# Performance work log

Hardware: AMD Instinct MI355X
Metric: run time of the kernel (lower is better)

## Reference

```python
import jax, jax.numpy as jnp
from jax import lax
import numpy as np

B, L = 256, 4096
H, RL, RH = 128, 2, 32   # num_hiddens, residual layers, residual hiddens
K, D = 512, 64           # codebook size, embedding dim
CC = 0.25                # commitment cost


def conv1d(x, w, b=None, stride=1, pad=0, circular=False):
    # x: (N,C,L), w: (O,I,k)
    if circular and pad > 0:
        x = jnp.pad(x, ((0, 0), (0, 0), (pad, pad)), mode='wrap')
        pad = 0
    y = lax.conv_general_dilated(x, w, (stride,), [(pad, pad)],
                                 dimension_numbers=('NCH', 'OIH', 'NCH'))
    return y if b is None else y + b[None, :, None]


def convt1d(x, w, b):
    # PyTorch ConvTranspose1d(k=4, s=2, p=1); w: (I,O,4). out_len = 2*L.
    wt = jnp.flip(jnp.swapaxes(w, 0, 1), -1)  # (O,I,4)
    y = lax.conv_general_dilated(x, wt, (1,), [(2, 2)], lhs_dilation=(2,),
                                 dimension_numbers=('NCH', 'OIH', 'NCH'))
    return y + b[None, :, None]


def res_stack(x, w1s, w2s):
    for i in range(w1s.shape[0]):
        h = conv1d(jax.nn.relu(x), w1s[i], None, 1, 1, circular=True)
        h = conv1d(jax.nn.relu(h), w2s[i], None, 1, 0)
        x = x + h
    return jax.nn.relu(x)


def setup_inputs() -> dict:
    key = jax.random.key(0)
    ks = iter(jax.random.split(key, 64))

    def w(*shape):
        fan_in = int(np.prod(shape[1:]))
        return jax.random.normal(next(ks), shape, jnp.float32) / np.sqrt(fan_in)

    def bias(n):
        return jax.random.uniform(next(ks), (n,), jnp.float32, -0.05, 0.05)

    inp = {'x': jax.random.normal(next(ks), (B, 1, L), jnp.float32)}
    # Encoder
    inp['enc_c1_w'] = w(H // 2, 1, 4);      inp['enc_c1_b'] = bias(H // 2)
    inp['enc_c2_w'] = w(H, H // 2, 4);      inp['enc_c2_b'] = bias(H)
    inp['enc_c3_w'] = w(H, H, 4);           inp['enc_c3_b'] = bias(H)
    inp['enc_c4_w'] = w(H, H, 4);           inp['enc_c4_b'] = bias(H)
    inp['enc_cf_w'] = w(H, H, 3);           inp['enc_cf_b'] = bias(H)
    inp['enc_res_w1'] = w(RL, RH, H, 3)
    inp['enc_res_w2'] = w(RL, H, RH, 1)
    # pre-VQ 1x1 conv
    inp['prevq_w'] = w(D, H, 1);            inp['prevq_b'] = bias(D)
    # codebook: uniform(-1/K, 1/K) as in source
    inp['emb'] = jax.random.uniform(next(ks), (K, D), jnp.float32, -1.0 / K, 1.0 / K)
    # Decoder
    inp['dec_init_w'] = w(H, D, 3);         inp['dec_init_b'] = bias(H)
    inp['dec_res_w1'] = w(RL, RH, H, 3)
    inp['dec_res_w2'] = w(RL, H, RH, 1)
    inp['ct0_w'] = w(H, H, 4);              inp['ct0_b'] = bias(H)
    inp['ct1_w'] = w(H, H, 4);              inp['ct1_b'] = bias(H)
    inp['ct2_w'] = w(H, H // 2, 4);         inp['ct2_b'] = bias(H // 2)
    inp['ct3_w'] = w(H // 2, 1, 4);         inp['ct3_b'] = bias(1)
    return inp


def _forward(x, enc_c1_w, enc_c1_b, enc_c2_w, enc_c2_b, enc_c3_w, enc_c3_b,
             enc_c4_w, enc_c4_b, enc_cf_w, enc_cf_b, enc_res_w1, enc_res_w2,
             prevq_w, prevq_b, emb, dec_init_w, dec_init_b, dec_res_w1,
             dec_res_w2, ct0_w, ct0_b, ct1_w, ct1_b, ct2_w, ct2_b, ct3_w, ct3_b):
    sg = lax.stop_gradient
    relu = jax.nn.relu
    # ---- Encoder (circular padding) ----
    z = relu(conv1d(x, enc_c1_w, enc_c1_b, 2, 1, circular=True))
    z = relu(conv1d(z, enc_c2_w, enc_c2_b, 2, 1, circular=True))
    z = relu(conv1d(z, enc_c3_w, enc_c3_b, 2, 1, circular=True))
    z = relu(conv1d(z, enc_c4_w, enc_c4_b, 2, 1, circular=True))
    z = conv1d(z, enc_cf_w, enc_cf_b, 1, 1, circular=True)
    z = res_stack(z, enc_res_w1, enc_res_w2)
    z = conv1d(z, prevq_w, prevq_b, 1, 0)        # (B, D, T)
    # ---- Vector quantizer ----
    z_t = jnp.transpose(z, (0, 2, 1))            # (B, T, D)
    flat = z_t.reshape(-1, D)                    # (BT, D)
    dist = (jnp.sum(flat ** 2, axis=1, keepdims=True)
            + jnp.sum(emb ** 2, axis=1)
            - 2.0 * flat @ emb.T)                # (BT, K)
    idx = jnp.argmin(dist, axis=1)               # (BT,)
    enc = jax.nn.one_hot(idx, K, dtype=flat.dtype)
    q = (enc @ emb).reshape(z_t.shape)           # (B, T, D)
    e_loss = jnp.mean((sg(q) - z_t) ** 2)
    q_loss = jnp.mean((q - sg(z_t)) ** 2)
    loss = q_loss + CC * e_loss
    q_st = z_t + sg(q - z_t)                     # straight-through
    avg = jnp.mean(enc, axis=0)
    perplexity = jnp.exp(-jnp.sum(avg * jnp.log(avg + 1e-10)))
    quantized = jnp.transpose(q_st, (0, 2, 1))   # (B, D, T)
    # ---- Decoder ----
    h = conv1d(quantized, dec_init_w, dec_init_b, 1, 1)
    h = res_stack(h, dec_res_w1, dec_res_w2)
    h = relu(convt1d(h, ct0_w, ct0_b))
    h = relu(convt1d(h, ct1_w, ct1_b))
    h = relu(convt1d(h, ct2_w, ct2_b))
    x_recon = convt1d(h, ct3_w, ct3_b)           # (B, 1, L)
    return loss, x_recon, perplexity


def reference(x, enc_c1_w, enc_c1_b, enc_c2_w, enc_c2_b, enc_c3_w, enc_c3_b,
              enc_c4_w, enc_c4_b, enc_cf_w, enc_cf_b, enc_res_w1, enc_res_w2,
              prevq_w, prevq_b, emb, dec_init_w, dec_init_b, dec_res_w1,
              dec_res_w2, ct0_w, ct0_b, ct1_w, ct1_b, ct2_w, ct2_b, ct3_w, ct3_b):
    return _forward(x, enc_c1_w, enc_c1_b, enc_c2_w, enc_c2_b, enc_c3_w,
                    enc_c3_b, enc_c4_w, enc_c4_b, enc_cf_w, enc_cf_b,
                    enc_res_w1, enc_res_w2, prevq_w, prevq_b, emb,
                    dec_init_w, dec_init_b, dec_res_w1, dec_res_w2,
                    ct0_w, ct0_b, ct1_w, ct1_b, ct2_w, ct2_b, ct3_w, ct3_b)
```

## Files before the change

### kernel.cpp

```cpp
#include <hip/hip_runtime.h>

#define DEVI __device__ __forceinline__

typedef __bf16 bf16x8 __attribute__((ext_vector_type(8)));
typedef float f32x4 __attribute__((ext_vector_type(4)));

DEVI ushort f2b(float f) {
  uint b = __float_as_uint(f);
  uint r = (b + 0x7FFFu + ((b >> 16) & 1u)) >> 16;
  return (ushort)r;
}
DEVI float b2f(ushort u) { return __uint_as_float(((uint)u) << 16); }

struct PrepArgs {
  int nw;
  int tot[20];
  const float* src[20];
  ushort* dst[20];
  int ci[20], co[20], sco[20], sci[20], sk[20];
};

__global__ __launch_bounds__(256)
void prep_all(PrepArgs a, int total) {
  int i = blockIdx.x * 256 + threadIdx.x;
  if (i >= total) return;
  int w = 0;
  while (i >= a.tot[w]) { i -= a.tot[w]; ++w; }
  const int li = i;
  const int CI = a.ci[w];
  int ciX = i % CI;
  int rest = i / CI;
  int coX = rest % a.co[w];
  int k = rest / a.co[w];
  a.dst[w][li] = f2b(a.src[w][coX * a.sco[w] + ciX * a.sci[w] + k * a.sk[w]]);
}

__global__ __launch_bounds__(256)
void enc1_bf(const float* __restrict__ x, const float* __restrict__ w1,
             const float* __restrict__ b1, ushort* __restrict__ out) {
  __shared__ float xl[516];
  __shared__ float w1s[256];
  __shared__ float b1s[64];
  const int n = blockIdx.x >> 3;
  const int t0 = (blockIdx.x & 7) << 8;
  const int tid = threadIdx.x;
  const float* xb = x + ((size_t)n << 12);
  for (int j = tid; j < 514; j += 256)
    xl[j] = xb[(2 * t0 - 1 + j + 4096) & 4095];
  if (tid < 256) w1s[tid] = w1[tid];
  if (tid < 64) b1s[tid] = b1[tid];
  __syncthreads();

  const int oct = tid & 7;
  float4 w4[8];
  float bs[8];
  #pragma unroll
  for (int e = 0; e < 8; ++e) {
    w4[e] = *reinterpret_cast<const float4*>(&w1s[(oct * 8 + e) * 4]);
    bs[e] = b1s[oct * 8 + e];
  }
  ushort* ob = out + (((size_t)n * 2048 + t0) << 6) + tid * 8;
  #pragma unroll
  for (int it = 0; it < 8; ++it) {
    const int tl = it * 32 + (tid >> 3);
    const float x0 = xl[2 * tl], x1 = xl[2 * tl + 1], x2 = xl[2 * tl + 2], x3 = xl[2 * tl + 3];
    uint pack[4];
    #pragma unroll
    for (int h = 0; h < 4; ++h) {
      float s0 = fmaf(w4[2 * h].x, x0, fmaf(w4[2 * h].y, x1,
                 fmaf(w4[2 * h].z, x2, fmaf(w4[2 * h].w, x3, bs[2 * h]))));
      float s1 = fmaf(w4[2 * h + 1].x, x0, fmaf(w4[2 * h + 1].y, x1,
                 fmaf(w4[2 * h + 1].z, x2, fmaf(w4[2 * h + 1].w, x3, bs[2 * h + 1]))));
      pack[h] = (uint)f2b(fmaxf(s0, 0.0f)) | ((uint)f2b(fmaxf(s1, 0.0f)) << 16);
    }
    *reinterpret_cast<uint4*>(ob + it * 2048) = uint4{pack[0], pack[1], pack[2], pack[3]};
  }
}

template<int CI, int CO, int K, int S, bool CIRC, bool GATHER, int NT, int WAVES_CO>
__global__ __launch_bounds__(256)
void conv_mfma(const ushort* __restrict__ in, const ushort* __restrict__ wb,
               const float* __restrict__ bias, const ushort* __restrict__ resid,
               ushort* __restrict__ out, const int* __restrict__ gidx,
               int Tin, int in_relu, int out_relu) {
  constexpr int PAD = (K > 1) ? 1 : 0;
  constexpr int TT = NT * 16;
  constexpr int SPAN = S * (TT - 1) + K;
  constexpr int CIG = CI / 8;
  constexpr int COT = CO / 16;
  constexpr int WCOT = COT / WAVES_CO;
  constexpr int WAVES_T = 4 / WAVES_CO;
  constexpr int WTT = NT / WAVES_T;
  constexpr int KSH = (S == 2) ? 1 : 0;
  static_assert(CI % 32 == 0 && COT % WAVES_CO == 0 && NT % WAVES_T == 0, "");

  __shared__ __align__(16) ushort xs[SPAN * CI];

  const int Tout = Tin / S;
  const int tilesPerB = Tout / TT;
  const int n = blockIdx.x / tilesPerB;
  const int t0 = (blockIdx.x % tilesPerB) * TT;
  const int tid = threadIdx.x;
  const int wid = tid >> 6, lane = tid & 63;
  const int l15 = lane & 15, l4 = lane >> 4;

  const int t_in0 = S * t0 - PAD;
  const ushort* inb = GATHER ? in : in + (size_t)n * Tin * CI;
  for (int i = tid; i < SPAN * CIG; i += 256) {
    int t = i / CIG, g = i - (i / CIG) * CIG;
    int tg = t_in0 + t;
    uint4 v;
    if (CIRC) {
      tg = (tg < 0) ? tg + Tin : (tg >= Tin ? tg - Tin : tg);
      v = *reinterpret_cast<const uint4*>(inb + (size_t)tg * CI + g * 8);
    } else if (GATHER) {
      if ((unsigned)tg < (unsigned)Tin) {
        int id = gidx[n * Tin + tg];
        v = *reinterpret_cast<const uint4*>(inb + (size_t)id * CI + g * 8);
      } else
        v = uint4{0, 0, 0, 0};
    } else {
      if ((unsigned)tg < (unsigned)Tin)
        v = *reinterpret_cast<const uint4*>(inb + (size_t)tg * CI + g * 8);
      else
        v = uint4{0, 0, 0, 0};
    }
    if (in_relu) {
      ushort* pv = reinterpret_cast<ushort*>(&v);
      #pragma unroll
      for (int e = 0; e < 8; ++e) pv[e] = (pv[e] & 0x8000) ? 0 : pv[e];
    }
    *reinterpret_cast<uint4*>(&xs[t * CI + ((g ^ ((t >> KSH) & (CIG - 1))) * 8)]) = v;
  }
  __syncthreads();

  const int wco = wid % WAVES_CO;
  const int wt = wid / WAVES_CO;
  const int co_base = wco * WCOT * 16;
  const int t_base = wt * WTT * 16;

  f32x4 acc[WTT][WCOT] = {};

  for (int cc = 0; cc < CI / 32; ++cc) {
    bf16x8 bk[K][WCOT];
    #pragma unroll
    for (int k = 0; k < K; ++k)
      #pragma unroll
      for (int c = 0; c < WCOT; ++c)
        bk[k][c] = __builtin_bit_cast(bf16x8, *reinterpret_cast<const uint4*>(
            wb + (size_t)((k * CO + co_base + c * 16 + l15)) * CI + cc * 32 + l4 * 8));
    #pragma unroll
    for (int k = 0; k < K; ++k) {
      #pragma unroll
      for (int tt2 = 0; tt2 < WTT; ++tt2) {
        int trow = S * (t_base + tt2 * 16 + l15) + k;
        int g = cc * 4 + l4;
        bf16x8 afr = __builtin_bit_cast(bf16x8, *reinterpret_cast<const uint4*>(
            &xs[trow * CI + ((g ^ ((trow >> KSH) & (CIG - 1))) * 8)]));
        #pragma unroll
        for (int c = 0; c < WCOT; ++c)
          acc[tt2][c] = __builtin_amdgcn_mfma_f32_16x16x32_bf16(afr, bk[k][c], acc[tt2][c], 0, 0, 0);
      }
    }
  }

  float bv[WCOT];
  #pragma unroll
  for (int c = 0; c < WCOT; ++c)
    bv[c] = bias ? bias[co_base + c * 16 + l15] : 0.0f;
  ushort* outb = out + (size_t)n * Tout * CO;
  const ushort* resb = resid ? resid + (size_t)n * Tout * CO : nullptr;
  #pragma unroll
  for (int tt2 = 0; tt2 < WTT; ++tt2)
    #pragma unroll
    for (int c = 0; c < WCOT; ++c)
      #pragma unroll
      for (int r = 0; r < 4; ++r) {
        int t = t0 + t_base + tt2 * 16 + 4 * l4 + r;
        int co = co_base + c * 16 + l15;
        float v = acc[tt2][c][r] + bv[c];
        if (resb) v += b2f(resb[(size_t)t * CO + co]);
        if (out_relu) v = fmaxf(v, 0.0f);
        outb[(size_t)t * CO + co] = f2b(v);
      }
}

__global__ __launch_bounds__(256)
void res_mfma(const ushort* __restrict__ in, const ushort* __restrict__ wb1,
              const ushort* __restrict__ wb2, ushort* __restrict__ out) {
  constexpr int CI = 128, CIG = 16;
  constexpr int TT = 64, SPAN = 66, Tin = 256;
  __shared__ __align__(16) ushort xs[SPAN * CI];
  __shared__ __align__(16) ushort hs[TT][40];
  const int n = blockIdx.x >> 2;
  const int t0 = (blockIdx.x & 3) * TT;
  const int tid = threadIdx.x;
  const int wid = tid >> 6, lane = tid & 63;
  const int l15 = lane & 15, l4 = lane >> 4;
  const int t_in0 = t0 - 1;
  const ushort* inb = in + (size_t)n * Tin * CI;

  for (int i = tid; i < SPAN * CIG; i += 256) {
    int t = i >> 4, g = i & 15;
    int tg = t_in0 + t;
    tg = (tg < 0) ? tg + Tin : (tg >= Tin ? tg - Tin : tg);
    uint4 v = *reinterpret_cast<const uint4*>(inb + (size_t)tg * CI + g * 8);
    ushort* pv = reinterpret_cast<ushort*>(&v);
    #pragma unroll
    for (int e = 0; e < 8; ++e) pv[e] = (pv[e] & 0x8000) ? 0 : pv[e];
    *reinterpret_cast<uint4*>(&xs[t * CI + ((g ^ (t & 15)) * 8)]) = v;
  }
  __syncthreads();

  {
    f32x4 acc[2] = {};
    for (int cc = 0; cc < 4; ++cc)
      #pragma unroll
      for (int k = 0; k < 3; ++k) {
        bf16x8 bfr[2];
        #pragma unroll
        for (int c = 0; c < 2; ++c)
          bfr[c] = __builtin_bit_cast(bf16x8, *reinterpret_cast<const uint4*>(
              wb1 + (size_t)((k * 32 + c * 16 + l15)) * CI + cc * 32 + l4 * 8));
        int trow = wid * 16 + l15 + k;
        int g = cc * 4 + l4;
        bf16x8 afr = __builtin_bit_cast(bf16x8, *reinterpret_cast<const uint4*>(
            &xs[trow * CI + ((g ^ (trow & 15)) * 8)]));
        acc[0] = __builtin_amdgcn_mfma_f32_16x16x32_bf16(afr, bfr[0], acc[0], 0, 0, 0);
        acc[1] = __builtin_amdgcn_mfma_f32_16x16x32_bf16(afr, bfr[1], acc[1], 0, 0, 0);
      }
    #pragma unroll
    for (int c = 0; c < 2; ++c)
      #pragma unroll
      for (int r = 0; r < 4; ++r) {
        float v = acc[c][r];
        hs[wid * 16 + l4 * 4 + r][c * 16 + l15] = (v > 0.0f) ? f2b(v) : (ushort)0;
      }
  }
  __syncthreads();

  {
    bf16x8 afr = *reinterpret_cast<const bf16x8*>(&hs[wid * 16 + l15][l4 * 8]);
    f32x4 acc[8];
    #pragma unroll
    for (int c = 0; c < 8; ++c) {
      bf16x8 bfr = __builtin_bit_cast(bf16x8, *reinterpret_cast<const uint4*>(
          wb2 + (size_t)(c * 16 + l15) * 32 + l4 * 8));
      f32x4 z = {};
      acc[c] = __builtin_amdgcn_mfma_f32_16x16x32_bf16(afr, bfr, z, 0, 0, 0);
    }
    ushort* outb = out + (size_t)n * Tin * CI;
    #pragma unroll
    for (int c = 0; c < 8; ++c)
      #pragma unroll
      for (int r = 0; r < 4; ++r) {
        int t = t0 + wid * 16 + l4 * 4 + r;
        int co = c * 16 + l15;
        float v = acc[c][r] + b2f(inb[(size_t)t * CI + co]);
        outb[(size_t)t * CI + co] = f2b(v);
      }
  }
}

template<int CO>
__global__ __launch_bounds__(256)
void convt_mfma(const ushort* __restrict__ in, const ushort* __restrict__ wb,
                const float* __restrict__ bias, ushort* __restrict__ out,
                int Tin, int in_relu, int out_relu) {
  constexpr int CI = 128, CIG = 16;
  constexpr int NT = 4, TT = 64;
  constexpr int SPAN = TT + 2;
  constexpr int COT = CO / 16;
  constexpr int WCOT = (COT + 3) / 4;
  constexpr int WAVES_CO = COT / WCOT;
  constexpr int WTT = NT;

  __shared__ __align__(16) ushort xs[SPAN * CI];

  const int Tout = 2 * Tin;
  const int tilesPerB = Tin / TT;
  const int n = blockIdx.x / tilesPerB;
  const int tp0 = (blockIdx.x % tilesPerB) * TT;
  const int tid = threadIdx.x;
  const int wid = tid >> 6, lane = tid & 63;
  const int l15 = lane & 15, l4 = lane >> 4;

  const int t_in0 = tp0 - 1;
  const ushort* inb = in + (size_t)n * Tin * CI;
  for (int i = tid; i < SPAN * CIG; i += 256) {
    int t = i >> 4, g = i & 15;
    int tg = t_in0 + t;
    uint4 v;
    if ((unsigned)tg < (unsigned)Tin)
      v = *reinterpret_cast<const uint4*>(inb + (size_t)tg * CI + g * 8);
    else
      v = uint4{0, 0, 0, 0};
    if (in_relu) {
      ushort* pv = reinterpret_cast<ushort*>(&v);
      #pragma unroll
      for (int e = 0; e < 8; ++e) pv[e] = (pv[e] & 0x8000) ? 0 : pv[e];
    }
    *reinterpret_cast<uint4*>(&xs[t * CI + ((g ^ (t & 15)) * 8)]) = v;
  }
  __syncthreads();

  const int wco = wid % WAVES_CO;
  const int co_base = wco * WCOT * 16;

  f32x4 accE[WTT][WCOT] = {};
  f32x4 accO[WTT][WCOT] = {};

  for (int cc = 0; cc < 4; ++cc) {
    bf16x8 bk[4][WCOT];
    #pragma unroll
    for (int k = 0; k < 4; ++k)
      #pragma unroll
      for (int c = 0; c < WCOT; ++c)
        bk[k][c] = __builtin_bit_cast(bf16x8, *reinterpret_cast<const uint4*>(
            wb + (size_t)((k * CO + co_base + c * 16 + l15)) * CI + cc * 32 + l4 * 8));
    #pragma unroll
    for (int tt2 = 0; tt2 < WTT; ++tt2) {
      int lt = tt2 * 16 + l15 + 1;
      int g = cc * 4 + l4;
      bf16x8 a0 = __builtin_bit_cast(bf16x8, *reinterpret_cast<const uint4*>(
          &xs[lt * CI + ((g ^ (lt & 15)) * 8)]));
      bf16x8 am = __builtin_bit_cast(bf16x8, *reinterpret_cast<const uint4*>(
          &xs[(lt - 1) * CI + ((g ^ ((lt - 1) & 15)) * 8)]));
      bf16x8 ap = __builtin_bit_cast(bf16x8, *reinterpret_cast<const uint4*>(
          &xs[(lt + 1) * CI + ((g ^ ((lt + 1) & 15)) * 8)]));
      #pragma unroll
      for (int c = 0; c < WCOT; ++c) {
        accE[tt2][c] = __builtin_amdgcn_mfma_f32_16x16x32_bf16(a0, bk[1][c], accE[tt2][c], 0, 0, 0);
        accE[tt2][c] = __builtin_amdgcn_mfma_f32_16x16x32_bf16(am, bk[3][c], accE[tt2][c], 0, 0, 0);
        accO[tt2][c] = __builtin_amdgcn_mfma_f32_16x16x32_bf16(ap, bk[0][c], accO[tt2][c], 0, 0, 0);
        accO[tt2][c] = __builtin_amdgcn_mfma_f32_16x16x32_bf16(a0, bk[2][c], accO[tt2][c], 0, 0, 0);
      }
    }
  }

  float bv[WCOT];
  #pragma unroll
  for (int c = 0; c < WCOT; ++c) bv[c] = bias[co_base + c * 16 + l15];
  ushort* outb = out + (size_t)n * Tout * CO;
  #pragma unroll
  for (int tt2 = 0; tt2 < WTT; ++tt2)
    #pragma unroll
    for (int c = 0; c < WCOT; ++c)
      #pragma unroll
      for (int r = 0; r < 4; ++r) {
        int tp = tp0 + tt2 * 16 + 4 * l4 + r;
        int co = co_base + c * 16 + l15;
        float vE = accE[tt2][c][r] + bv[c];
        float vO = accO[tt2][c][r] + bv[c];
        if (out_relu) { vE = fmaxf(vE, 0.0f); vO = fmaxf(vO, 0.0f); }
        outb[(size_t)(2 * tp) * CO + co] = f2b(vE);
        outb[(size_t)(2 * tp + 1) * CO + co] = f2b(vO);
      }
}

__global__ __launch_bounds__(256)
void ct23_mfma(const ushort* __restrict__ in, const ushort* __restrict__ wb,
               const float* __restrict__ bias, const float* __restrict__ w3,
               const float* __restrict__ b3, float* __restrict__ out) {
  constexpr int CI = 128, CO = 64, CIG = 16;
  constexpr int TT = 64, SPAN = 66, Tin = 1024;
  __shared__ __align__(16) ushort xs[SPAN * CI];
  __shared__ ushort ys[64 * 134];
  __shared__ float w3s[256];

  const int n = blockIdx.x >> 4;
  const int tp0 = (blockIdx.x & 15) * TT;
  const int tid = threadIdx.x;
  const int wid = tid >> 6, lane = tid & 63;
  const int l15 = lane & 15, l4 = lane >> 4;
  const int t_in0 = tp0 - 1;
  const ushort* inb = in + (size_t)n * Tin * CI;

  if (tid < 256) w3s[tid] = w3[tid];
  for (int i = tid; i < SPAN * CIG; i += 256) {
    int t = i >> 4, g = i & 15;
    int tg = t_in0 + t;
    uint4 v;
    if ((unsigned)tg < (unsigned)Tin)
      v = *reinterpret_cast<const uint4*>(inb + (size_t)tg * CI + g * 8);
    else
      v = uint4{0, 0, 0, 0};
    *reinterpret_cast<uint4*>(&xs[t * CI + ((g ^ (t & 15)) * 8)]) = v;
  }
  __syncthreads();

  const int co_base = wid * 16;
  f32x4 accE[4] = {}, accO[4] = {};
  f32x4 hO = {}, hE = {};

  for (int cc = 0; cc < 4; ++cc) {
    bf16x8 bk[4];
    #pragma unroll
    for (int k = 0; k < 4; ++k)
      bk[k] = __builtin_bit_cast(bf16x8, *reinterpret_cast<const uint4*>(
          wb + (size_t)((k * CO + co_base + l15)) * CI + cc * 32 + l4 * 8));
    const int g = cc * 4 + l4;
    auto rd = [&](int lt) -> bf16x8 {
      return __builtin_bit_cast(bf16x8, *reinterpret_cast<const uint4*>(
          &xs[lt * CI + ((g ^ (lt & 15)) * 8)]));
    };
    #pragma unroll
    for (int tt2 = 0; tt2 < 4; ++tt2) {
      int lt = tt2 * 16 + l15 + 1;
      bf16x8 a0 = rd(lt), am = rd(lt - 1), ap = rd(lt + 1);
      accE[tt2] = __builtin_amdgcn_mfma_f32_16x16x32_bf16(a0, bk[1], accE[tt2], 0, 0, 0);
      accE[tt2] = __builtin_amdgcn_mfma_f32_16x16x32_bf16(am, bk[3], accE[tt2], 0, 0, 0);
      accO[tt2] = __builtin_amdgcn_mfma_f32_16x16x32_bf16(ap, bk[0], accO[tt2], 0, 0, 0);
      accO[tt2] = __builtin_amdgcn_mfma_f32_16x16x32_bf16(a0, bk[2], accO[tt2], 0, 0, 0);
    }
    bf16x8 h0 = rd(0), h1 = rd(1), h64 = rd(64), h65 = rd(65);
    hO = __builtin_amdgcn_mfma_f32_16x16x32_bf16(h1, bk[0], hO, 0, 0, 0);
    hO = __builtin_amdgcn_mfma_f32_16x16x32_bf16(h0, bk[2], hO, 0, 0, 0);
    hE = __builtin_amdgcn_mfma_f32_16x16x32_bf16(h65, bk[1], hE, 0, 0, 0);
    hE = __builtin_amdgcn_mfma_f32_16x16x32_bf16(h64, bk[3], hE, 0, 0, 0);
  }

  const float bv = bias[co_base + l15];
  ushort* yrow = &ys[(co_base + l15) * 134];
  #pragma unroll
  for (int tt2 = 0; tt2 < 4; ++tt2)
    #pragma unroll
    for (int r = 0; r < 4; ++r) {
      int m = tt2 * 16 + 4 * l4 + r;
      yrow[2 * m + 1] = f2b(fmaxf(accE[tt2][r] + bv, 0.0f));
      yrow[2 * m + 2] = f2b(fmaxf(accO[tt2][r] + bv, 0.0f));
    }
  if (l4 == 0) {
    yrow[0]   = (tp0 == 0) ? (ushort)0 : f2b(fmaxf(hO[0] + bv, 0.0f));
    yrow[129] = (tp0 + TT == Tin) ? (ushort)0 : f2b(fmaxf(hE[0] + bv, 0.0f));
  }
  __syncthreads();

  const int o = 4 * tp0 + tid;
  const int odd = o & 1;
  const int ga = odd ? ((o + 1) >> 1) : (o >> 1);
  const int gb = odd ? ((o - 1) >> 1) : (o / 2 - 1);
  const int ka = odd ? 0 : 1;
  const int kb = odd ? 2 : 3;
  const int ja = ga - (2 * tp0 - 1), jb = gb - (2 * tp0 - 1);
  float s = b3[0];
  #pragma unroll 16
  for (int ci = 0; ci < 64; ++ci) {
    s = fmaf(w3s[ci * 4 + ka], b2f(ys[ci * 134 + ja]), s);
    s = fmaf(w3s[ci * 4 + kb], b2f(ys[ci * 134 + jb]), s);
  }
  out[(size_t)n * 4096 + o] = s;
}

__global__ __launch_bounds__(256)
void vq_mfma(const ushort* __restrict__ zt, const ushort* __restrict__ embb,
             int* __restrict__ idx, int* __restrict__ hist,
             float* __restrict__ loss_accum) {
  __shared__ __align__(16) ushort es[512 * 64];
  __shared__ float eel[512];
  __shared__ int lhist[512];
  const int tid = threadIdx.x;
  const int wid = tid >> 6, lane = tid & 63;
  const int l15 = lane & 15, l4 = lane >> 4;

  for (int i = tid; i < 512 * 8; i += 256) {
    int c = i >> 3, g = i & 7;
    uint4 v = reinterpret_cast<const uint4*>(embb)[i];
    reinterpret_cast<uint4*>(es)[c * 8 + (g ^ (c & 7))] = v;
    const ushort* pv = reinterpret_cast<const ushort*>(&v);
    float ss = 0.0f;
    #pragma unroll
    for (int e = 0; e < 8; ++e) { float f = b2f(pv[e]); ss = fmaf(f, f, ss); }
    ss += __shfl_xor(ss, 1);
    ss += __shfl_xor(ss, 2);
    ss += __shfl_xor(ss, 4);
    if ((i & 7) == 0) eel[c] = ss;
  }
  for (int i = tid; i < 512; i += 256) lhist[i] = 0;
  __syncthreads();

  const int rb = blockIdx.x * 256 + wid * 64;
  bf16x8 bz[4][2];
  float zz[4], best[4];
  int bi[4];
  #pragma unroll
  for (int rt = 0; rt < 4; ++rt) {
    const int r = rb + rt * 16 + l15;
    uint4 v0 = *reinterpret_cast<const uint4*>(zt + (size_t)r * 64 + l4 * 8);
    uint4 v1 = *reinterpret_cast<const uint4*>(zt + (size_t)r * 64 + 32 + l4 * 8);
    bz[rt][0] = __builtin_bit_cast(bf16x8, v0);
    bz[rt][1] = __builtin_bit_cast(bf16x8, v1);
    float s = 0.0f;
    const ushort* p0 = reinterpret_cast<const ushort*>(&v0);
    const ushort* p1 = reinterpret_cast<const ushort*>(&v1);
    #pragma unroll
    for (int e = 0; e < 8; ++e) {
      float f0 = b2f(p0[e]), f1 = b2f(p1[e]);
      s = fmaf(f0, f0, fmaf(f1, f1, s));
    }
    s += __shfl_xor(s, 16);
    s += __shfl_xor(s, 32);
    zz[rt] = s;
    best[rt] = 3.4e38f;
    bi[rt] = 0;
  }

  for (int ct = 0; ct < 32; ++ct) {
    const int c = ct * 16 + l15;
    bf16x8 a0 = __builtin_bit_cast(bf16x8, reinterpret_cast<const uint4*>(es)[
        c * 8 + (l4 ^ (c & 7))]);
    bf16x8 a1 = __builtin_bit_cast(bf16x8, reinterpret_cast<const uint4*>(es)[
        c * 8 + ((4 | l4) ^ (c & 7))]);
    #pragma unroll
    for (int rt = 0; rt < 4; ++rt) {
      f32x4 acc = {};
      acc = __builtin_amdgcn_mfma_f32_16x16x32_bf16(a0, bz[rt][0], acc, 0, 0, 0);
      acc = __builtin_amdgcn_mfma_f32_16x16x32_bf16(a1, bz[rt][1], acc, 0, 0, 0);
      #pragma unroll
      for (int rr = 0; rr < 4; ++rr) {
        int code = ct * 16 + l4 * 4 + rr;
        float d = eel[code] - 2.0f * acc[rr];
        if (d < best[rt] || (d == best[rt] && code < bi[rt])) { best[rt] = d; bi[rt] = code; }
      }
    }
  }
  float vsum = 0.0f;
  #pragma unroll
  for (int rt = 0; rt < 4; ++rt) {
    #pragma unroll
    for (int m = 16; m <= 32; m <<= 1) {
      float ob = __shfl_xor(best[rt], m);
      int oi = __shfl_xor(bi[rt], m);
      if (ob < best[rt] || (ob == best[rt] && oi < bi[rt])) { best[rt] = ob; bi[rt] = oi; }
    }
    if (l4 == 0) {
      idx[rb + rt * 16 + l15] = bi[rt];
      atomicAdd(&lhist[bi[rt]], 1);
      vsum += zz[rt] + best[rt];
    }
  }
  #pragma unroll
  for (int m = 1; m < 64; m <<= 1) vsum += __shfl_xor(vsum, m);
  if (lane == 0) atomicAdd(loss_accum, vsum);
  __syncthreads();
  for (int i = tid; i < 512; i += 256)
    if (lhist[i]) atomicAdd(&hist[i], lhist[i]);
}

__global__ __launch_bounds__(512)
void finalize(const int* __restrict__ hist, const float* __restrict__ loss_accum,
              float* __restrict__ out) {
  __shared__ float red[8];
  int tid = threadIdx.x;
  float avg = (float)hist[tid] * (1.0f / 65536.0f);
  float v = avg * logf(avg + 1e-10f);
  for (int off = 32; off > 0; off >>= 1) v += __shfl_down(v, off);
  if ((tid & 63) == 0) red[tid >> 6] = v;
  __syncthreads();
  if (tid == 0) {
    float s = 0.0f;
    for (int i = 0; i < 8; ++i) s += red[i];
    out[1048577] = expf(-s);
    out[0] = 1.25f * loss_accum[0] * (1.0f / (65536.0f * 64.0f));
  }
}

extern "C" void kernel_launch(void* const* d_in, const int* in_sizes, int n_in,
                              void* d_out, int out_size, void* d_ws, size_t ws_size,
                              hipStream_t stream) {
  (void)in_sizes; (void)n_in; (void)out_size; (void)ws_size;
  const float* x    = (const float*)d_in[0];
  const float* c1w  = (const float*)d_in[1];
  const float* c1b  = (const float*)d_in[2];
  const float* c2w  = (const float*)d_in[3];
  const float* c2b  = (const float*)d_in[4];
  const float* c3w  = (const float*)d_in[5];
  const float* c3b  = (const float*)d_in[6];
  const float* c4w  = (const float*)d_in[7];
  const float* c4b  = (const float*)d_in[8];
  const float* cfw  = (const float*)d_in[9];
  const float* cfb  = (const float*)d_in[10];
  const float* erw1 = (const float*)d_in[11];
  const float* erw2 = (const float*)d_in[12];
  const float* pqw  = (const float*)d_in[13];
  const float* pqb  = (const float*)d_in[14];
  const float* emb  = (const float*)d_in[15];
  const float* diw  = (const float*)d_in[16];
  const float* dib  = (const float*)d_in[17];
  const float* drw1 = (const float*)d_in[18];
  const float* drw2 = (const float*)d_in[19];
  const float* t0w  = (const float*)d_in[20];
  const float* t0b  = (const float*)d_in[21];
  const float* t1w  = (const float*)d_in[22];
  const float* t1b  = (const float*)d_in[23];
  const float* t2w  = (const float*)d_in[24];
  const float* t2b  = (const float*)d_in[25];
  const float* t3w  = (const float*)d_in[26];
  const float* t3b  = (const float*)d_in[27];

  char* wsb = (char*)d_ws;
  ushort* R0 = (ushort*)wsb;
  ushort* R1 = (ushort*)(wsb + 67108864);
  ushort* R2 = (ushort*)(wsb + 134217728);
  ushort* R3 = (ushort*)(wsb + 0);
  ushort* R4 = (ushort*)(wsb + 16777216);
  ushort* R6 = (ushort*)(wsb + 37748736);
  ushort* WPu = (ushort*)(wsb + 167772160);
  ushort* wb_e2 = WPu + 0;
  ushort* wb_e3 = WPu + 32768;
  ushort* wb_e4 = WPu + 98304;
  ushort* wb_cf = WPu + 163840;
  ushort* wb_r1a = WPu + 212992;
  ushort* wb_r1b = WPu + 225280;
  ushort* wb_r2a = WPu + 237568;
  ushort* wb_r2b = WPu + 241664;
  ushort* wb_pq = WPu + 245760;
  ushort* wb_di = WPu + 253952;
  ushort* wb_d1a = WPu + 278528;
  ushort* wb_d1b = WPu + 290816;
  ushort* wb_d2a = WPu + 303104;
  ushort* wb_d2b = WPu + 307200;
  ushort* wb_t0 = WPu + 311296;
  ushort* wb_t1 = WPu + 376832;
  ushort* wb_t2 = WPu + 442368;
  ushort* wb_emb = WPu + 475136;
  char* fp = wsb + 167772160 + 1048576;
  int*   idxb  = (int*)(fp + 2048);
  int*   histb = (int*)(fp + 2048 + 262144);
  float* lossb = (float*)(fp + 2048 + 262144 + 2048);
  float* outp  = (float*)d_out;

  hipMemsetAsync(histb, 0, 512 * sizeof(int), stream);
  hipMemsetAsync(lossb, 0, sizeof(float), stream);

  PrepArgs pa{};
  int nw = 0, total = 0;
  auto addw = [&](const float* src, ushort* dst, int CO, int CI, int K,
                  int sco, int sci, int sk) {
    pa.tot[nw] = K * CO * CI; pa.src[nw] = src; pa.dst[nw] = dst;
    pa.ci[nw] = CI; pa.co[nw] = CO; pa.sco[nw] = sco; pa.sci[nw] = sci; pa.sk[nw] = sk;
    total += pa.tot[nw]; ++nw;
  };
  addw(c2w, wb_e2, 128, 64, 4, 256, 4, 1);
  addw(c3w, wb_e3, 128, 128, 4, 512, 4, 1);
  addw(c4w, wb_e4, 128, 128, 4, 512, 4, 1);
  addw(cfw, wb_cf, 128, 128, 3, 384, 3, 1);
  addw(erw1, wb_r1a, 32, 128, 3, 384, 3, 1);
  addw(erw1 + 12288, wb_r1b, 32, 128, 3, 384, 3, 1);
  addw(erw2, wb_r2a, 128, 32, 1, 32, 1, 1);
  addw(erw2 + 4096, wb_r2b, 128, 32, 1, 32, 1, 1);
  addw(pqw, wb_pq, 64, 128, 1, 128, 1, 1);
  addw(diw, wb_di, 128, 64, 3, 192, 3, 1);
  addw(drw1, wb_d1a, 32, 128, 3, 384, 3, 1);
  addw(drw1 + 12288, wb_d1b, 32, 128, 3, 384, 3, 1);
  addw(drw2, wb_d2a, 128, 32, 1, 32, 1, 1);
  addw(drw2 + 4096, wb_d2b, 128, 32, 1, 32, 1, 1);
  addw(t0w, wb_t0, 128, 128, 4, 4, 512, 1);
  addw(t1w, wb_t1, 128, 128, 4, 4, 512, 1);
  addw(t2w, wb_t2, 64, 128, 4, 4, 256, 1);
  addw(emb, wb_emb, 512, 64, 1, 64, 1, 1);
  pa.nw = nw;
  prep_all<<<(total + 255) / 256, 256, 0, stream>>>(pa, total);

  enc1_bf<<<2048, 256, 0, stream>>>(x, c1w, c1b, R0);
  conv_mfma<64, 128, 4, 2, true, false, 4, 4><<<4096, 256, 0, stream>>>(R0, wb_e2, c2b, nullptr, R1, nullptr, 2048, 0, 1);
  conv_mfma<128, 128, 4, 2, true, false, 4, 4><<<2048, 256, 0, stream>>>(R1, wb_e3, c3b, nullptr, R2, nullptr, 1024, 0, 1);
  conv_mfma<128, 128, 4, 2, true, false, 4, 4><<<1024, 256, 0, stream>>>(R2, wb_e4, c4b, nullptr, R3, nullptr, 512, 0, 1);
  conv_mfma<128, 128, 3, 1, true, false, 8, 2><<<512, 256, 0, stream>>>(R3, wb_cf, cfb, nullptr, R4, nullptr, 256, 0, 0);
  res_mfma<<<1024, 256, 0, stream>>>(R4, wb_r1a, wb_r2a, R3);
  res_mfma<<<1024, 256, 0, stream>>>(R3, wb_r1b, wb_r2b, R4);
  conv_mfma<128, 64, 1, 1, false, false, 8, 2><<<512, 256, 0, stream>>>(R4, wb_pq, pqb, nullptr, R6, nullptr, 256, 1, 0);
  vq_mfma<<<256, 256, 0, stream>>>(R6, wb_emb, idxb, histb, lossb);
  finalize<<<1, 512, 0, stream>>>(histb, lossb, outp);
  conv_mfma<64, 128, 3, 1, false, true, 8, 2><<<512, 256, 0, stream>>>(wb_emb, wb_di, dib, nullptr, R3, idxb, 256, 0, 0);
  res_mfma<<<1024, 256, 0, stream>>>(R3, wb_d1a, wb_d2a, R4);
  res_mfma<<<1024, 256, 0, stream>>>(R4, wb_d1b, wb_d2b, R3);
  convt_mfma<128><<<1024, 256, 0, stream>>>(R3, wb_t0, t0b, R2, 256, 1, 1);
  convt_mfma<128><<<2048, 256, 0, stream>>>(R2, wb_t1, t1b, R0, 512, 0, 1);
  ct23_mfma<<<4096, 256, 0, stream>>>(R0, wb_t2, t2b, t3w, t3b, outp + 1);
}
```

Before: 446.3 us.

## Cut shared memory via channel-chunked conv staging and LDS buffer aliasing

Adds an NCHUNK template parameter to conv_mfma so the input tile is staged into LDS in channel halves, used for the two stride-2 encoder convs. This halves their shared-memory footprint, which should allow more resident blocks per CU, at the cost of an extra barrier and reload pass. res_mfma and ct23_mfma reuse the input staging buffer for intermediate results. ct23 also transposes its intermediate layout and uses pre-split weights so the final 64-tap dot product reads packed bf16 pairs.

```diff
diff --git a/kernel.cpp b/kernel.cpp
--- a/kernel.cpp
+++ b/kernel.cpp
@@ -77,7 +77,8 @@
   }
 }
 
-template<int CI, int CO, int K, int S, bool CIRC, bool GATHER, int NT, int WAVES_CO>
+template<int CI, int CO, int K, int S, bool CIRC, bool GATHER, int NT, int WAVES_CO,
+         int NCHUNK = 1>
 __global__ __launch_bounds__(256)
 void conv_mfma(const ushort* __restrict__ in, const ushort* __restrict__ wb,
                const float* __restrict__ bias, const ushort* __restrict__ resid,
@@ -86,15 +87,16 @@
   constexpr int PAD = (K > 1) ? 1 : 0;
   constexpr int TT = NT * 16;
   constexpr int SPAN = S * (TT - 1) + K;
-  constexpr int CIG = CI / 8;
+  constexpr int CICH = CI / NCHUNK;
+  constexpr int CIGc = CICH / 8;
   constexpr int COT = CO / 16;
   constexpr int WCOT = COT / WAVES_CO;
   constexpr int WAVES_T = 4 / WAVES_CO;
   constexpr int WTT = NT / WAVES_T;
   constexpr int KSH = (S == 2) ? 1 : 0;
-  static_assert(CI % 32 == 0 && COT % WAVES_CO == 0 && NT % WAVES_T == 0, "");
-
-  __shared__ __align__(16) ushort xs[SPAN * CI];
+  static_assert(CICH % 32 == 0 && COT % WAVES_CO == 0 && NT % WAVES_T == 0, "");
+
+  __shared__ __align__(16) ushort xs[SPAN * CICH];
 
   const int Tout = Tin / S;
   const int tilesPerB = Tout / TT;
@@ -106,33 +108,6 @@
 
   const int t_in0 = S * t0 - PAD;
   const ushort* inb = GATHER ? in : in + (size_t)n * Tin * CI;
-  for (int i = tid; i < SPAN * CIG; i += 256) {
-    int t = i / CIG, g = i - (i / CIG) * CIG;
-    int tg = t_in0 + t;
-    uint4 v;
-    if (CIRC) {
-      tg = (tg < 0) ? tg + Tin : (tg >= Tin ? tg - Tin : tg);
-      v = *reinterpret_cast<const uint4*>(inb + (size_t)tg * CI + g * 8);
-    } else if (GATHER) {
-      if ((unsigned)tg < (unsigned)Tin) {
-        int id = gidx[n * Tin + tg];
-        v = *reinterpret_cast<const uint4*>(inb + (size_t)id * CI + g * 8);
-      } else
-        v = uint4{0, 0, 0, 0};
-    } else {
-      if ((unsigned)tg < (unsigned)Tin)
-        v = *reinterpret_cast<const uint4*>(inb + (size_t)tg * CI + g * 8);
-      else
-        v = uint4{0, 0, 0, 0};
-    }
-    if (in_relu) {
-      ushort* pv = reinterpret_cast<ushort*>(&v);
-      #pragma unroll
-      for (int e = 0; e < 8; ++e) pv[e] = (pv[e] & 0x8000) ? 0 : pv[e];
-    }
-    *reinterpret_cast<uint4*>(&xs[t * CI + ((g ^ ((t >> KSH) & (CIG - 1))) * 8)]) = v;
-  }
-  __syncthreads();
 
   const int wco = wid % WAVES_CO;
   const int wt = wid / WAVES_CO;
@@ -141,25 +116,57 @@
 
   f32x4 acc[WTT][WCOT] = {};
 
-  for (int cc = 0; cc < CI / 32; ++cc) {
-    bf16x8 bk[K][WCOT];
-    #pragma unroll
-    for (int k = 0; k < K; ++k)
-      #pragma unroll
-      for (int c = 0; c < WCOT; ++c)
-        bk[k][c] = __builtin_bit_cast(bf16x8, *reinterpret_cast<const uint4*>(
-            wb + (size_t)((k * CO + co_base + c * 16 + l15)) * CI + cc * 32 + l4 * 8));
-    #pragma unroll
-    for (int k = 0; k < K; ++k) {
-      #pragma unroll
-      for (int tt2 = 0; tt2 < WTT; ++tt2) {
-        int trow = S * (t_base + tt2 * 16 + l15) + k;
-        int g = cc * 4 + l4;
-        bf16x8 afr = __builtin_bit_cast(bf16x8, *reinterpret_cast<const uint4*>(
-            &xs[trow * CI + ((g ^ ((trow >> KSH) & (CIG - 1))) * 8)]));
+  for (int h = 0; h < NCHUNK; ++h) {
+    if (h) __syncthreads();
+    for (int i = tid; i < SPAN * CIGc; i += 256) {
+      int t = i / CIGc, g = i - (i / CIGc) * CIGc;
+      int tg = t_in0 + t;
+      uint4 v;
+      if (CIRC) {
+        tg = (tg < 0) ? tg + Tin : (tg >= Tin ? tg - Tin : tg);
+        v = *reinterpret_cast<const uint4*>(inb + (size_t)tg * CI + h * CICH + g * 8);
+      } else if (GATHER) {
+        if ((unsigned)tg < (unsigned)Tin) {
+          int id = gidx[n * Tin + tg];
+          v = *reinterpret_cast<const uint4*>(inb + (size_t)id * CI + h * CICH + g * 8);
+        } else
+          v = uint4{0, 0, 0, 0};
+      } else {
+        if ((unsigned)tg < (unsigned)Tin)
+          v = *reinterpret_cast<const uint4*>(inb + (size_t)tg * CI + h * CICH + g * 8);
+        else
+          v = uint4{0, 0, 0, 0};
+      }
+      if (in_relu) {
+        ushort* pv = reinterpret_cast<ushort*>(&v);
+        #pragma unroll
+        for (int e = 0; e < 8; ++e) pv[e] = (pv[e] & 0x8000) ? 0 : pv[e];
+      }
+      *reinterpret_cast<uint4*>(&xs[t * CICH + ((g ^ ((t >> KSH) & (CIGc - 1))) * 8)]) = v;
+    }
+    __syncthreads();
+
+    for (int cc = 0; cc < CICH / 32; ++cc) {
+      const int ccg = h * (CICH / 32) + cc;
+      bf16x8 bk[K][WCOT];
+      #pragma unroll
+      for (int k = 0; k < K; ++k)
         #pragma unroll
         for (int c = 0; c < WCOT; ++c)
-          acc[tt2][c] = __builtin_amdgcn_mfma_f32_16x16x32_bf16(afr, bk[k][c], acc[tt2][c], 0, 0, 0);
+          bk[k][c] = __builtin_bit_cast(bf16x8, *reinterpret_cast<const uint4*>(
+              wb + (size_t)((k * CO + co_base + c * 16 + l15)) * CI + ccg * 32 + l4 * 8));
+      #pragma unroll
+      for (int k = 0; k < K; ++k) {
+        #pragma unroll
+        for (int tt2 = 0; tt2 < WTT; ++tt2) {
+          int trow = S * (t_base + tt2 * 16 + l15) + k;
+          int g = cc * 4 + l4;
+          bf16x8 afr = __builtin_bit_cast(bf16x8, *reinterpret_cast<const uint4*>(
+              &xs[trow * CICH + ((g ^ ((trow >> KSH) & (CIGc - 1))) * 8)]));
+          #pragma unroll
+          for (int c = 0; c < WCOT; ++c)
+            acc[tt2][c] = __builtin_amdgcn_mfma_f32_16x16x32_bf16(afr, bk[k][c], acc[tt2][c], 0, 0, 0);
+        }
       }
     }
   }
@@ -191,7 +198,7 @@
   constexpr int CI = 128, CIG = 16;
   constexpr int TT = 64, SPAN = 66, Tin = 256;
   __shared__ __align__(16) ushort xs[SPAN * CI];
-  __shared__ __align__(16) ushort hs[TT][40];
+  ushort* hs = xs;
   const int n = blockIdx.x >> 2;
   const int t0 = (blockIdx.x & 3) * TT;
   const int tid = threadIdx.x;
@@ -212,35 +219,34 @@
   }
   __syncthreads();
 
+  f32x4 acc1[2] = {};
+  for (int cc = 0; cc < 4; ++cc)
+    #pragma unroll
+    for (int k = 0; k < 3; ++k) {
+      bf16x8 bfr[2];
+      #pragma unroll
+      for (int c = 0; c < 2; ++c)
+        bfr[c] = __builtin_bit_cast(bf16x8, *reinterpret_cast<const uint4*>(
+            wb1 + (size_t)((k * 32 + c * 16 + l15)) * CI + cc * 32 + l4 * 8));
+      int trow = wid * 16 + l15 + k;
+      int g = cc * 4 + l4;
+      bf16x8 afr = __builtin_bit_cast(bf16x8, *reinterpret_cast<const uint4*>(
+          &xs[trow * CI + ((g ^ (trow & 15)) * 8)]));
+      acc1[0] = __builtin_amdgcn_mfma_f32_16x16x32_bf16(afr, bfr[0], acc1[0], 0, 0, 0);
+      acc1[1] = __builtin_amdgcn_mfma_f32_16x16x32_bf16(afr, bfr[1], acc1[1], 0, 0, 0);
+    }
+  __syncthreads();
+  #pragma unroll
+  for (int c = 0; c < 2; ++c)
+    #pragma unroll
+    for (int r = 0; r < 4; ++r) {
+      float v = acc1[c][r];
+      hs[(wid * 16 + l4 * 4 + r) * 40 + c * 16 + l15] = (v > 0.0f) ? f2b(v) : (ushort)0;
+    }
+  __syncthreads();
+
   {
-    f32x4 acc[2] = {};
-    for (int cc = 0; cc < 4; ++cc)
-      #pragma unroll
-      for (int k = 0; k < 3; ++k) {
-        bf16x8 bfr[2];
-        #pragma unroll
-        for (int c = 0; c < 2; ++c)
-          bfr[c] = __builtin_bit_cast(bf16x8, *reinterpret_cast<const uint4*>(
-              wb1 + (size_t)((k * 32 + c * 16 + l15)) * CI + cc * 32 + l4 * 8));
-        int trow = wid * 16 + l15 + k;
-        int g = cc * 4 + l4;
-        bf16x8 afr = __builtin_bit_cast(bf16x8, *reinterpret_cast<const uint4*>(
-            &xs[trow * CI + ((g ^ (trow & 15)) * 8)]));
-        acc[0] = __builtin_amdgcn_mfma_f32_16x16x32_bf16(afr, bfr[0], acc[0], 0, 0, 0);
-        acc[1] = __builtin_amdgcn_mfma_f32_16x16x32_bf16(afr, bfr[1], acc[1], 0, 0, 0);
-      }
-    #pragma unroll
-    for (int c = 0; c < 2; ++c)
-      #pragma unroll
-      for (int r = 0; r < 4; ++r) {
-        float v = acc[c][r];
-        hs[wid * 16 + l4 * 4 + r][c * 16 + l15] = (v > 0.0f) ? f2b(v) : (ushort)0;
-      }
-  }
-  __syncthreads();
-
-  {
-    bf16x8 afr = *reinterpret_cast<const bf16x8*>(&hs[wid * 16 + l15][l4 * 8]);
+    bf16x8 afr = *reinterpret_cast<const bf16x8*>(&hs[(wid * 16 + l15) * 40 + l4 * 8]);
     f32x4 acc[8];
     #pragma unroll
     for (int c = 0; c < 8; ++c) {
@@ -364,9 +370,10 @@
                const float* __restrict__ b3, float* __restrict__ out) {
   constexpr int CI = 128, CO = 64, CIG = 16;
   constexpr int TT = 64, SPAN = 66, Tin = 1024;
-  __shared__ __align__(16) ushort xs[SPAN * CI];
-  __shared__ ushort ys[64 * 134];
-  __shared__ float w3s[256];
+  __shared__ __align__(16) ushort buf[8580];
+  __shared__ float2 w3p[2][64];
+  ushort* xs = buf;
+  ushort* ys = buf;
 
   const int n = blockIdx.x >> 4;
   const int tp0 = (blockIdx.x & 15) * TT;
@@ -376,7 +383,12 @@
   const int t_in0 = tp0 - 1;
   const ushort* inb = in + (size_t)n * Tin * CI;
 
-  if (tid < 256) w3s[tid] = w3[tid];
+  if (tid < 128) {
+    int parity = tid >> 6, ci = tid & 63;
+    w3p[parity][ci] = parity
+        ? float2{w3[ci * 4 + 0], w3[ci * 4 + 2]}
+        : float2{w3[ci * 4 + 1], w3[ci * 4 + 3]};
+  }
   for (int i = tid; i < SPAN * CIG; i += 256) {
     int t = i >> 4, g = i & 15;
     int tg = t_in0 + t;
@@ -389,7 +401,7 @@
   }
   __syncthreads();
 
-  const int co_base = wid * 16;
+  const int co = wid * 16 + l15;
   f32x4 accE[4] = {}, accO[4] = {};
   f32x4 hO = {}, hE = {};
 
@@ -398,7 +410,7 @@
     #pragma unroll
     for (int k = 0; k < 4; ++k)
       bk[k] = __builtin_bit_cast(bf16x8, *reinterpret_cast<const uint4*>(
-          wb + (size_t)((k * CO + co_base + l15)) * CI + cc * 32 + l4 * 8));
+          wb + (size_t)((k * CO + co)) * CI + cc * 32 + l4 * 8));
     const int g = cc * 4 + l4;
     auto rd = [&](int lt) -> bf16x8 {
       return __builtin_bit_cast(bf16x8, *reinterpret_cast<const uint4*>(
@@ -419,35 +431,39 @@
     hE = __builtin_amdgcn_mfma_f32_16x16x32_bf16(h65, bk[1], hE, 0, 0, 0);
     hE = __builtin_amdgcn_mfma_f32_16x16x32_bf16(h64, bk[3], hE, 0, 0, 0);
   }
-
-  const float bv = bias[co_base + l15];
-  ushort* yrow = &ys[(co_base + l15) * 134];
+  __syncthreads();
+
+  const float bv = bias[co];
   #pragma unroll
   for (int tt2 = 0; tt2 < 4; ++tt2)
     #pragma unroll
     for (int r = 0; r < 4; ++r) {
       int m = tt2 * 16 + 4 * l4 + r;
-      yrow[2 * m + 1] = f2b(fmaxf(accE[tt2][r] + bv, 0.0f));
-      yrow[2 * m + 2] = f2b(fmaxf(accO[tt2][r] + bv, 0.0f));
+      ys[(2 * m + 1) * 66 + co] = f2b(fmaxf(accE[tt2][r] + bv, 0.0f));
+      ys[(2 * m + 2) * 66 + co] = f2b(fmaxf(accO[tt2][r] + bv, 0.0f));
     }
   if (l4 == 0) {
-    yrow[0]   = (tp0 == 0) ? (ushort)0 : f2b(fmaxf(hO[0] + bv, 0.0f));
-    yrow[129] = (tp0 + TT == Tin) ? (ushort)0 : f2b(fmaxf(hE[0] + bv, 0.0f));
+    ys[co]            = (tp0 == 0) ? (ushort)0 : f2b(fmaxf(hO[0] + bv, 0.0f));
+    ys[129 * 66 + co] = (tp0 + TT == Tin) ? (ushort)0 : f2b(fmaxf(hE[0] + bv, 0.0f));
   }
   __syncthreads();
 
   const int o = 4 * tp0 + tid;
-  const int odd = o & 1;
-  const int ga = odd ? ((o + 1) >> 1) : (o >> 1);
-  const int gb = odd ? ((o - 1) >> 1) : (o / 2 - 1);
-  const int ka = odd ? 0 : 1;
-  const int kb = odd ? 2 : 3;
-  const int ja = ga - (2 * tp0 - 1), jb = gb - (2 * tp0 - 1);
+  const int odd = tid & 1;
+  const int ha = (tid + odd) >> 1;
+  const ushort* ra = &ys[(ha + 1) * 66];
+  const ushort* rb = &ys[ha * 66];
+  const float2* wp = w3p[odd];
   float s = b3[0];
-  #pragma unroll 16
-  for (int ci = 0; ci < 64; ++ci) {
-    s = fmaf(w3s[ci * 4 + ka], b2f(ys[ci * 134 + ja]), s);
-    s = fmaf(w3s[ci * 4 + kb], b2f(ys[ci * 134 + jb]), s);
+  #pragma unroll
+  for (int c = 0; c < 32; ++c) {
+    uint va = *reinterpret_cast<const uint*>(ra + 2 * c);
+    uint vb = *reinterpret_cast<const uint*>(rb + 2 * c);
+    float2 w0 = wp[2 * c], w1 = wp[2 * c + 1];
+    s = fmaf(w0.x, __uint_as_float(va << 16), s);
+    s = fmaf(w1.x, __uint_as_float(va & 0xFFFF0000u), s);
+    s = fmaf(w0.y, __uint_as_float(vb << 16), s);
+    s = fmaf(w1.y, __uint_as_float(vb & 0xFFFF0000u), s);
   }
   out[(size_t)n * 4096 + o] = s;
 }
@@ -664,8 +680,8 @@
 
   enc1_bf<<<2048, 256, 0, stream>>>(x, c1w, c1b, R0);
   conv_mfma<64, 128, 4, 2, true, false, 4, 4><<<4096, 256, 0, stream>>>(R0, wb_e2, c2b, nullptr, R1, nullptr, 2048, 0, 1);
-  conv_mfma<128, 128, 4, 2, true, false, 4, 4><<<2048, 256, 0, stream>>>(R1, wb_e3, c3b, nullptr, R2, nullptr, 1024, 0, 1);
-  conv_mfma<128, 128, 4, 2, true, false, 4, 4><<<1024, 256, 0, stream>>>(R2, wb_e4, c4b, nullptr, R3, nullptr, 512, 0, 1);
+  conv_mfma<128, 128, 4, 2, true, false, 4, 4, 2><<<2048, 256, 0, stream>>>(R1, wb_e3, c3b, nullptr, R2, nullptr, 1024, 0, 1);
+  conv_mfma<128, 128, 4, 2, true, false, 4, 4, 2><<<1024, 256, 0, stream>>>(R2, wb_e4, c4b, nullptr, R3, nullptr, 512, 0, 1);
   conv_mfma<128, 128, 3, 1, true, false, 8, 2><<<512, 256, 0, stream>>>(R3, wb_cf, cfb, nullptr, R4, nullptr, 256, 0, 0);
   res_mfma<<<1024, 256, 0, stream>>>(R4, wb_r1a, wb_r2a, R3);
   res_mfma<<<1024, 256, 0, stream>>>(R3, wb_r1b, wb_r2b, R4);
```

New measurement: 442.5 us. Within noise of the previous version (-0.8%).
